# Kernel optimization log

Measured on AMD Instinct MI355X. Metric: run time of the kernel, lower is better.

The kernel has to match this reference:

```python
import jax, jax.numpy as jnp
import numpy as np

HEADS = 16  # matches init_kwargs


def setup_inputs() -> dict:
    key = jax.random.key(0)
    ks = jax.random.split(key, 9)
    N, L, E, D = 2, 2048, 1024, 64
    return {
        "query": jax.random.normal(ks[0], (N, L, E), dtype=jnp.float32),
        "keys": jax.random.normal(ks[1], (N, L, E), dtype=jnp.float32),
        "values": jax.random.normal(ks[2], (N, L, E), dtype=jnp.float32),
        "masks": jax.random.randint(ks[3], (N, 1, 1, L), 0, 2, dtype=jnp.int32),
        "Wq": jax.random.normal(ks[4], (D, D), dtype=jnp.float32) / np.sqrt(D),
        "Wk": jax.random.normal(ks[5], (D, D), dtype=jnp.float32) / np.sqrt(D),
        "Wv": jax.random.normal(ks[6], (D, D), dtype=jnp.float32) / np.sqrt(D),
        "Wo": jax.random.normal(ks[7], (E, E), dtype=jnp.float32) / np.sqrt(E),
        "bo": jax.random.normal(ks[8], (E,), dtype=jnp.float32),
    }


def reference(query, keys, values, masks, Wq, Wk, Wv, Wo, bo):
    N, Lq, E = query.shape
    Lk = keys.shape[1]
    H = HEADS
    D = E // H
    # split heads: [N, L, H, D]
    q = query.reshape(N, Lq, H, D)
    k = keys.reshape(N, Lk, H, D)
    v = values.reshape(N, Lk, H, D)
    # per-head linear projections (weights shared across heads); Linear: x @ W.T
    q = jnp.einsum("nqhd,ed->nqhe", q, Wq)
    k = jnp.einsum("nkhd,ed->nkhe", k, Wk)
    v = jnp.einsum("nkhd,ed->nkhe", v, Wv)
    # scores [N, H, Lq, Lk]
    scores = jnp.einsum("nqhd,nkhd->nhqk", q, k)
    scores = jnp.where(masks == 0, jnp.float32(-1e20), scores)
    # NOTE: original scales by sqrt(embed_size), not sqrt(head_dim)
    attn = jax.nn.softmax(scores / jnp.sqrt(jnp.float32(E)), axis=3)
    out = jnp.einsum("nhqk,nkhd->nqhd", attn, v).reshape(N, Lq, E)
    return out @ Wo.T + bo
```

## Files before the change

kernel.cpp:

```cpp
#include <hip/hip_runtime.h>


typedef __bf16 bf16_t;
typedef __bf16 bf16x4 __attribute__((ext_vector_type(4)));
typedef __bf16 bf16x8 __attribute__((ext_vector_type(8)));
typedef float f32x4 __attribute__((ext_vector_type(4)));

#define MFMA16(a, b, c) __builtin_amdgcn_mfma_f32_16x16x32_bf16((a), (b), (c), 0, 0, 0)

#define GLOAD_LDS16(gp, lp)                                              \
    __builtin_amdgcn_global_load_lds(                                    \
        (const __attribute__((address_space(1))) void*)(gp),             \
        (__attribute__((address_space(3))) void*)(lp), 16, 0, 0)

__device__ inline bf16x8 cvt8(const float* __restrict__ p, float scale) {
    f32x4 a = *(const f32x4*)p;
    f32x4 b = *(const f32x4*)(p + 4);
    bf16x8 r;
    r[0] = (bf16_t)(a[0] * scale); r[1] = (bf16_t)(a[1] * scale);
    r[2] = (bf16_t)(a[2] * scale); r[3] = (bf16_t)(a[3] * scale);
    r[4] = (bf16_t)(b[0] * scale); r[5] = (bf16_t)(b[1] * scale);
    r[6] = (bf16_t)(b[2] * scale); r[7] = (bf16_t)(b[3] * scale);
    return r;
}

__global__ __launch_bounds__(256) void scan_kernel(const int* __restrict__ msk,
                                                   int* __restrict__ excl)
{
    __shared__ int sums[256];
    const int t = threadIdx.x;
    for (int n = 0; n < 2; n++) {
        const int* m = msk + n * 2048;
        int* e = excl + n * 2049;
        int v[8], s = 0;
        #pragma unroll
        for (int j = 0; j < 8; j++) { v[j] = (m[t * 8 + j] != 0); s += v[j]; }
        sums[t] = s;
        __syncthreads();
        if (t == 0) {
            int a = 0;
            for (int i = 0; i < 256; i++) { int x = sums[i]; sums[i] = a; a += x; }
            e[2048] = a;
        }
        __syncthreads();
        int a = sums[t];
        #pragma unroll
        for (int j = 0; j < 8; j++) { e[t * 8 + j] = a; a += v[j]; }
        __syncthreads();
    }
}

__global__ __launch_bounds__(256) void qkv_proj_kernel(
    const float* __restrict__ qin, const float* __restrict__ kin,
    const float* __restrict__ vin,
    const float* __restrict__ Wq, const float* __restrict__ Wk,
    const float* __restrict__ Wv, const float* __restrict__ Wo,
    const int* __restrict__ excl,
    bf16_t* __restrict__ qp, bf16_t* __restrict__ kc, bf16_t* __restrict__ vcT,
    bf16_t* __restrict__ Wob)
{
    __shared__ __align__(16) char smem[51200];

    const int t = threadIdx.x;
    const int w = t >> 6, lane = t & 63, quad = lane >> 4, l16 = lane & 15;

    if (blockIdx.y == 3) {
        int idx = blockIdx.x * 1024 + t * 4;
        f32x4 v = *(const f32x4*)&Wo[idx];
        bf16x4 r;
        r[0] = (bf16_t)v[0]; r[1] = (bf16_t)v[1];
        r[2] = (bf16_t)v[2]; r[3] = (bf16_t)v[3];
        *(bf16x4*)&Wob[idx] = r;
        return;
    }

    if (blockIdx.y == 2) {
        bf16_t* Ct = (bf16_t*)smem;
        short* mapS = (short*)(smem + 16384);
        const int h = blockIdx.x & 15;
        const int tb = (blockIdx.x >> 4) * 64;
        const int n = tb >> 11, l0 = tb & 2047;
        const int tg = tb + w * 16 + l16;

        bf16x8 b0 = cvt8(&vin[(size_t)tg * 1024 + h * 64 + quad * 8], 1.0f);
        bf16x8 b1 = cvt8(&vin[(size_t)tg * 1024 + h * 64 + 32 + quad * 8], 1.0f);

        const int cbase = excl[n * 2049 + l0];
        const int cnt   = excl[n * 2049 + l0 + 64] - cbase;
        if (t < 64) {
            int c  = excl[n * 2049 + l0 + t];
            int c1 = excl[n * 2049 + l0 + t + 1];
            if (c1 > c) mapS[c - cbase] = (short)t;
        }

        #pragma unroll
        for (int nt = 0; nt < 4; nt++) {
            bf16x8 a0 = cvt8(&Wv[(nt * 16 + l16) * 64 + quad * 8], 1.0f);
            bf16x8 a1 = cvt8(&Wv[(nt * 16 + l16) * 64 + 32 + quad * 8], 1.0f);
            f32x4 acc = {0.f, 0.f, 0.f, 0.f};
            acc = MFMA16(a0, b0, acc);
            acc = MFMA16(a1, b1, acc);
            #pragma unroll
            for (int r = 0; r < 4; r++)
                Ct[(nt * 16 + quad * 4 + r) * 72 + w * 16 + l16] = (bf16_t)acc[r];
        }
        __syncthreads();
        const int p = t & 63, rg = t >> 6;
        if (p < cnt) {
            int j = mapS[p];
            size_t ob = ((size_t)(n * 16 + h)) * 131072 + cbase + p;
            #pragma unroll
            for (int rr = 0; rr < 16; rr++) {
                int r = rg * 16 + rr;
                vcT[ob + (size_t)r * 2048] = Ct[r * 72 + j];
            }
        }
        return;
    }

    if (blockIdx.x >= 512) return;
    const bool isK = (blockIdx.y == 1);
    const float* x; const float* W; float scale;
    if (!isK) { x = qin; W = Wq; scale = 0.03125f; }
    else      { x = kin; W = Wk; scale = 1.0f; }

    float* Xs = (float*)smem;
    bf16_t* Ct2 = (bf16_t*)(smem + 32768);

    const int g0 = blockIdx.x * 128;

    #pragma unroll
    for (int j = 0; j < 8; j++) {
        int br = w * 32 + j * 4;
        GLOAD_LDS16(&x[(size_t)(g0 + br) * 64 + lane * 4], &Xs[br * 64]);
    }
    __syncthreads();

    const int rbase = w * 32;
    bf16x8 a[2][2];
    #pragma unroll
    for (int qs = 0; qs < 2; qs++)
        #pragma unroll
        for (int c = 0; c < 2; c++)
            a[qs][c] = cvt8(&Xs[(rbase + qs * 16 + l16) * 64 + c * 32 + quad * 8], scale);

    f32x4 acc[4][2];
    #pragma unroll
    for (int nt = 0; nt < 4; nt++) {
        bf16x8 b0 = cvt8(&W[(nt * 16 + l16) * 64 + quad * 8], 1.0f);
        bf16x8 b1 = cvt8(&W[(nt * 16 + l16) * 64 + 32 + quad * 8], 1.0f);
        #pragma unroll
        for (int qs = 0; qs < 2; qs++) {
            f32x4 z = {0.f, 0.f, 0.f, 0.f};
            z = MFMA16(a[qs][0], b0, z);
            z = MFMA16(a[qs][1], b1, z);
            acc[nt][qs] = z;
        }
    }

    #pragma unroll
    for (int nt = 0; nt < 4; nt++)
        #pragma unroll
        for (int qs = 0; qs < 2; qs++)
            #pragma unroll
            for (int r = 0; r < 4; r++)
                Ct2[(rbase + qs * 16 + quad * 4 + r) * 72 + nt * 16 + l16] = (bf16_t)acc[nt][qs][r];
    __syncthreads();

    #pragma unroll
    for (int it = 0; it < 4; it++) {
        int j = it * 32 + (t >> 3);
        int g = g0 + j, h2 = g & 15, token = g >> 4;
        int n2 = token >> 11, l = token & 2047;
        bf16x8 val = *(const bf16x8*)&Ct2[j * 72 + (t & 7) * 8];
        if (isK) {
            int c  = excl[n2 * 2049 + l];
            int c1 = excl[n2 * 2049 + l + 1];
            if (c1 > c)
                *(bf16x8*)&kc[(((size_t)(n2 * 16 + h2)) * 2048 + c) * 64 + (t & 7) * 8] = val;
        } else {
            *(bf16x8*)&qp[(((size_t)(n2 * 16 + h2)) * 2048 + l) * 64 + (t & 7) * 8] = val;
        }
    }
}

__global__ __launch_bounds__(256) void attn_kernel(
    const bf16_t* __restrict__ qp, const bf16_t* __restrict__ kc,
    const bf16_t* __restrict__ vcT, const int* __restrict__ excl,
    bf16_t* __restrict__ ao)
{
    __shared__ bf16_t Kt[2][64][64];
    __shared__ bf16_t Vt[2][64][64];
    __shared__ bf16_t PwT[4][32][72];

    const int t = threadIdx.x;
    const int w = t >> 6, lane = t & 63, quad = lane >> 4, l16 = lane & 15;

    const int flat = blockIdx.x;
    const int xcd = flat & 7, slot = flat >> 3;
    const int nh = xcd * 4 + (slot >> 4), qb = slot & 15;
    const int n = nh >> 4, h = nh & 15;
    const int qbase = qb * 128 + w * 32;
    const size_t nhbase = (size_t)nh * 131072;

    const int Lc = excl[n * 2049 + 2048];
    const int ntiles = (Lc + 63) >> 6;

    bf16x8 aq[2][2];
    #pragma unroll
    for (int qs = 0; qs < 2; qs++)
        #pragma unroll
        for (int c = 0; c < 2; c++)
            aq[qs][c] = *(const bf16x8*)&qp[nhbase + (size_t)(qbase + qs * 16 + l16) * 64 + c * 32 + quad * 8];

    f32x4 o[2][4];
    float lsum[2] = {0.f, 0.f};
    #pragma unroll
    for (int qs = 0; qs < 2; qs++)
        #pragma unroll
        for (int dt = 0; dt < 4; dt++) {
            o[qs][dt][0] = 0.f; o[qs][dt][1] = 0.f; o[qs][dt][2] = 0.f; o[qs][dt][3] = 0.f;
        }

    const int kwbase = w * 16;

    #pragma unroll
    for (int j = 0; j < 2; j++) {
        int rb = kwbase + j * 8;
        GLOAD_LDS16(&kc[nhbase + (size_t)rb * 64 + lane * 8], &Kt[0][rb][0]);
        GLOAD_LDS16(&vcT[nhbase + (size_t)(rb + (lane >> 3)) * 2048 + (lane & 7) * 8],
                    &Vt[0][rb][0]);
    }

    for (int i = 0; i < ntiles; i++) {
        const int cb = i & 1, nb = cb ^ 1;
        const int k0 = i * 64;
        __syncthreads();

        if (i + 1 < ntiles) {
            const int kn = k0 + 64;
            #pragma unroll
            for (int j = 0; j < 2; j++) {
                int rb = kwbase + j * 8;
                GLOAD_LDS16(&kc[nhbase + (size_t)(kn + rb) * 64 + lane * 8], &Kt[nb][rb][0]);
                GLOAD_LDS16(&vcT[nhbase + (size_t)(rb + (lane >> 3)) * 2048 + kn + (lane & 7) * 8],
                            &Vt[nb][rb][0]);
            }
        }

        f32x4 st[2][4];
        #pragma unroll
        for (int ct = 0; ct < 4; ct++) {
            bf16x8 kb0 = *(const bf16x8*)&Kt[cb][ct * 16 + l16][quad * 8];
            bf16x8 kb1 = *(const bf16x8*)&Kt[cb][ct * 16 + l16][32 + quad * 8];
            #pragma unroll
            for (int qs = 0; qs < 2; qs++) {
                f32x4 acc = {0.f, 0.f, 0.f, 0.f};
                acc = MFMA16(kb0, aq[qs][0], acc);
                acc = MFMA16(kb1, aq[qs][1], acc);
                st[qs][ct] = acc;
            }
        }

        if (k0 + 64 <= Lc) {
            #pragma unroll
            for (int ct = 0; ct < 4; ct++)
                #pragma unroll
                for (int qs = 0; qs < 2; qs++) {
                    bf16x4 pk;
                    #pragma unroll
                    for (int r = 0; r < 4; r++) {
                        float p = __expf(st[qs][ct][r]);
                        lsum[qs] += p;
                        pk[r] = (bf16_t)p;
                    }
                    *(bf16x4*)&PwT[w][qs * 16 + l16][ct * 16 + quad * 4] = pk;
                }
        } else {
            #pragma unroll
            for (int ct = 0; ct < 4; ct++)
                #pragma unroll
                for (int qs = 0; qs < 2; qs++) {
                    bf16x4 pk;
                    #pragma unroll
                    for (int r = 0; r < 4; r++) {
                        int kk = k0 + ct * 16 + quad * 4 + r;
                        float p = (kk < Lc) ? __expf(st[qs][ct][r]) : 0.0f;
                        lsum[qs] += p;
                        pk[r] = (bf16_t)p;
                    }
                    *(bf16x4*)&PwT[w][qs * 16 + l16][ct * 16 + quad * 4] = pk;
                }
        }
        asm volatile("s_waitcnt lgkmcnt(0)" ::: "memory");

        bf16x8 bp[2][2];
        #pragma unroll
        for (int qs = 0; qs < 2; qs++) {
            bp[qs][0] = *(const bf16x8*)&PwT[w][qs * 16 + l16][quad * 8];
            bp[qs][1] = *(const bf16x8*)&PwT[w][qs * 16 + l16][32 + quad * 8];
        }
        #pragma unroll
        for (int dt = 0; dt < 4; dt++) {
            bf16x8 va0 = *(const bf16x8*)&Vt[cb][dt * 16 + l16][quad * 8];
            bf16x8 va1 = *(const bf16x8*)&Vt[cb][dt * 16 + l16][32 + quad * 8];
            #pragma unroll
            for (int qs = 0; qs < 2; qs++) {
                o[qs][dt] = MFMA16(va0, bp[qs][0], o[qs][dt]);
                o[qs][dt] = MFMA16(va1, bp[qs][1], o[qs][dt]);
            }
        }
    }

    #pragma unroll
    for (int qs = 0; qs < 2; qs++) {
        float v = lsum[qs];
        v += __shfl_xor(v, 16);
        v += __shfl_xor(v, 32);
        float inv = 1.0f / v;
        const int q = qbase + qs * 16 + l16;
        const size_t base = ((size_t)n * 2048 + q) * 1024 + h * 64;
        #pragma unroll
        for (int dt = 0; dt < 4; dt++) {
            bf16x4 ov;
            #pragma unroll
            for (int r = 0; r < 4; r++) ov[r] = (bf16_t)(o[qs][dt][r] * inv);
            *(bf16x4*)&ao[base + dt * 16 + quad * 4] = ov;
        }
    }
}

__global__ __launch_bounds__(256, 2) void out_proj_kernel(
    const bf16_t* __restrict__ X, const bf16_t* __restrict__ Wob,
    const float* __restrict__ bo, float* __restrict__ out)
{
    __shared__ bf16_t Xs[2][128][64];
    __shared__ bf16_t Ws[2][64][64];

    const int t = threadIdx.x;
    const int w = t >> 6, lane = t & 63, quad = lane >> 4, l16 = lane & 15;
    const int Mbase = blockIdx.x * 128;
    const int Nbase = blockIdx.y * 64;
    const int mrow = (w & 1) * 64;
    const int ncol = (w >> 1) * 32;

    f32x4 acc[4][2];
    #pragma unroll
    for (int mi = 0; mi < 4; mi++)
        #pragma unroll
        for (int ni = 0; ni < 2; ni++) {
            acc[mi][ni][0] = 0.f; acc[mi][ni][1] = 0.f;
            acc[mi][ni][2] = 0.f; acc[mi][ni][3] = 0.f;
        }

    #pragma unroll
    for (int j = 0; j < 4; j++) {
        int br = w * 32 + j * 8;
        GLOAD_LDS16(&X[(size_t)(Mbase + br + (lane >> 3)) * 1024 + (lane & 7) * 8],
                    &Xs[0][br][0]);
    }
    #pragma unroll
    for (int j = 0; j < 2; j++) {
        int br = w * 16 + j * 8;
        GLOAD_LDS16(&Wob[(size_t)(Nbase + br + (lane >> 3)) * 1024 + (lane & 7) * 8],
                    &Ws[0][br][0]);
    }

    for (int i = 0; i < 16; i++) {
        const int cb = i & 1, nb = cb ^ 1;
        __syncthreads();

        if (i < 15) {
            const int kn = (i + 1) * 64;
            #pragma unroll
            for (int j = 0; j < 4; j++) {
                int br = w * 32 + j * 8;
                GLOAD_LDS16(&X[(size_t)(Mbase + br + (lane >> 3)) * 1024 + kn + (lane & 7) * 8],
                            &Xs[nb][br][0]);
            }
            #pragma unroll
            for (int j = 0; j < 2; j++) {
                int br = w * 16 + j * 8;
                GLOAD_LDS16(&Wob[(size_t)(Nbase + br + (lane >> 3)) * 1024 + kn + (lane & 7) * 8],
                            &Ws[nb][br][0]);
            }
        }

        #pragma unroll
        for (int c = 0; c < 2; c++) {
            bf16x8 bfr[2];
            #pragma unroll
            for (int ni = 0; ni < 2; ni++)
                bfr[ni] = *(const bf16x8*)&Ws[cb][ncol + ni * 16 + l16][c * 32 + quad * 8];
            #pragma unroll
            for (int mi = 0; mi < 4; mi++) {
                bf16x8 afr = *(const bf16x8*)&Xs[cb][mrow + mi * 16 + l16][c * 32 + quad * 8];
                #pragma unroll
                for (int ni = 0; ni < 2; ni++)
                    acc[mi][ni] = MFMA16(afr, bfr[ni], acc[mi][ni]);
            }
        }
    }

    #pragma unroll
    for (int ni = 0; ni < 2; ni++) {
        float b = bo[Nbase + ncol + ni * 16 + l16];
        #pragma unroll
        for (int mi = 0; mi < 4; mi++) {
            #pragma unroll
            for (int r = 0; r < 4; r++) {
                int row = Mbase + mrow + mi * 16 + quad * 4 + r;
                out[(size_t)row * 1024 + Nbase + ncol + ni * 16 + l16] = acc[mi][ni][r] + b;
            }
        }
    }
}

extern "C" void kernel_launch(void* const* d_in, const int* in_sizes, int n_in,
                              void* d_out, int out_size, void* d_ws, size_t ws_size,
                              hipStream_t stream)
{
    const float* qin = (const float*)d_in[0];
    const float* kin = (const float*)d_in[1];
    const float* vin = (const float*)d_in[2];
    const int*   msk = (const int*)d_in[3];
    const float* Wq  = (const float*)d_in[4];
    const float* Wk  = (const float*)d_in[5];
    const float* Wv  = (const float*)d_in[6];
    const float* Wo  = (const float*)d_in[7];
    const float* bo  = (const float*)d_in[8];
    float* out = (float*)d_out;

    bf16_t* ws  = (bf16_t*)d_ws;
    bf16_t* qp  = ws;
    bf16_t* kc  = ws + 4194304;
    bf16_t* vcT = ws + 8388608;
    bf16_t* ao  = ws + 12582912;
    bf16_t* Wob = ws + 16777216;
    int* excl   = (int*)(ws + 17825792);

    scan_kernel<<<1, 256, 0, stream>>>(msk, excl);
    qkv_proj_kernel<<<dim3(1024, 4), 256, 0, stream>>>(qin, kin, vin, Wq, Wk, Wv, Wo,
                                                        excl, qp, kc, vcT, Wob);
    attn_kernel<<<dim3(512), 256, 0, stream>>>(qp, kc, vcT, excl, ao);
    out_proj_kernel<<<dim3(32, 16), 256, 0, stream>>>(ao, Wob, bo, out);
}
```

Measured before the change: 184.5 us.

## Keep softmax probabilities in registers via permlane swaps, use exp2, parallelize mask scan

The attention kernel no longer writes P through an LDS staging buffer. It packs probabilities to bf16 with v_cvt_pk_bf16_f32 and rearranges them across lane quads with permlane32/16 swaps so they can feed the PV MFMA directly. The Q scale now folds in log2(e), so raw v_exp_f32 (exp2) replaces __expf. The mask prefix-scan runs on one block per batch and uses a wave shuffle scan instead of a serial 256-element loop. The change removes LDS traffic and waits in the inner loop, but it depends on the permlane swaps reproducing the exact operand layout the MFMA expects.

```diff
diff --git a/kernel.cpp b/kernel.cpp
--- a/kernel.cpp
+++ b/kernel.cpp
@@ -5,6 +5,7 @@
 typedef __bf16 bf16x4 __attribute__((ext_vector_type(4)));
 typedef __bf16 bf16x8 __attribute__((ext_vector_type(8)));
 typedef float f32x4 __attribute__((ext_vector_type(4)));
+typedef unsigned int u32x4 __attribute__((ext_vector_type(4)));
 
 #define MFMA16(a, b, c) __builtin_amdgcn_mfma_f32_16x16x32_bf16((a), (b), (c), 0, 0, 0)
 
@@ -24,30 +25,54 @@
     return r;
 }
 
+__device__ inline float exp2_fast(float x) {
+    float r;
+    asm("v_exp_f32 %0, %1" : "=v"(r) : "v"(x));
+    return r;
+}
+
+__device__ inline unsigned cvt_pk_bf16(float lo, float hi) {
+    unsigned r;
+    asm("v_cvt_pk_bf16_f32 %0, %1, %2" : "=v"(r) : "v"(lo), "v"(hi));
+    return r;
+}
+
+__device__ inline void xchg_quads(unsigned &x, unsigned &y) {
+    asm("v_permlane32_swap_b32 %0, %1\n\t"
+        "v_permlane16_swap_b32 %0, %1"
+        : "+v"(x), "+v"(y));
+}
+
 __global__ __launch_bounds__(256) void scan_kernel(const int* __restrict__ msk,
                                                    int* __restrict__ excl)
 {
-    __shared__ int sums[256];
-    const int t = threadIdx.x;
-    for (int n = 0; n < 2; n++) {
-        const int* m = msk + n * 2048;
-        int* e = excl + n * 2049;
-        int v[8], s = 0;
-        #pragma unroll
-        for (int j = 0; j < 8; j++) { v[j] = (m[t * 8 + j] != 0); s += v[j]; }
-        sums[t] = s;
-        __syncthreads();
-        if (t == 0) {
-            int a = 0;
-            for (int i = 0; i < 256; i++) { int x = sums[i]; sums[i] = a; a += x; }
-            e[2048] = a;
-        }
-        __syncthreads();
-        int a = sums[t];
-        #pragma unroll
-        for (int j = 0; j < 8; j++) { e[t * 8 + j] = a; a += v[j]; }
-        __syncthreads();
-    }
+    __shared__ int wsum[4];
+    const int n = blockIdx.x;
+    const int t = threadIdx.x, lane = t & 63, w = t >> 6;
+    const int* m = msk + n * 2048;
+    int* e = excl + n * 2049;
+
+    int v[8], s = 0;
+    #pragma unroll
+    for (int j = 0; j < 8; j++) { v[j] = (m[t * 8 + j] != 0); s += v[j]; }
+
+    int inc = s;
+    #pragma unroll
+    for (int d = 1; d < 64; d <<= 1) {
+        int o = __shfl_up(inc, d);
+        if (lane >= d) inc += o;
+    }
+    if (lane == 63) wsum[w] = inc;
+    __syncthreads();
+    int off = 0;
+    #pragma unroll
+    for (int i = 0; i < 4; i++)
+        if (i < w) off += wsum[i];
+
+    int a = off + inc - s;
+    #pragma unroll
+    for (int j = 0; j < 8; j++) { e[t * 8 + j] = a; a += v[j]; }
+    if (t == 255) e[2048] = a;
 }
 
 __global__ __launch_bounds__(256) void qkv_proj_kernel(
@@ -121,7 +146,7 @@
     if (blockIdx.x >= 512) return;
     const bool isK = (blockIdx.y == 1);
     const float* x; const float* W; float scale;
-    if (!isK) { x = qin; W = Wq; scale = 0.03125f; }
+    if (!isK) { x = qin; W = Wq; scale = 0.04508422f; }
     else      { x = kin; W = Wk; scale = 1.0f; }
 
     float* Xs = (float*)smem;
@@ -191,7 +216,6 @@
 {
     __shared__ bf16_t Kt[2][64][64];
     __shared__ bf16_t Vt[2][64][64];
-    __shared__ bf16_t PwT[4][32][72];
 
     const int t = threadIdx.x;
     const int w = t >> 6, lane = t & 63, quad = lane >> 4, l16 = lane & 15;
@@ -264,42 +288,49 @@
 
         if (k0 + 64 <= Lc) {
             #pragma unroll
-            for (int ct = 0; ct < 4; ct++)
+            for (int qs = 0; qs < 2; qs++)
                 #pragma unroll
-                for (int qs = 0; qs < 2; qs++) {
-                    bf16x4 pk;
+                for (int ct = 0; ct < 4; ct++)
                     #pragma unroll
                     for (int r = 0; r < 4; r++) {
-                        float p = __expf(st[qs][ct][r]);
+                        float p = exp2_fast(st[qs][ct][r]);
                         lsum[qs] += p;
-                        pk[r] = (bf16_t)p;
+                        st[qs][ct][r] = p;
                     }
-                    *(bf16x4*)&PwT[w][qs * 16 + l16][ct * 16 + quad * 4] = pk;
-                }
         } else {
             #pragma unroll
-            for (int ct = 0; ct < 4; ct++)
+            for (int qs = 0; qs < 2; qs++)
                 #pragma unroll
-                for (int qs = 0; qs < 2; qs++) {
-                    bf16x4 pk;
+                for (int ct = 0; ct < 4; ct++)
                     #pragma unroll
                     for (int r = 0; r < 4; r++) {
                         int kk = k0 + ct * 16 + quad * 4 + r;
-                        float p = (kk < Lc) ? __expf(st[qs][ct][r]) : 0.0f;
+                        float p = (kk < Lc) ? exp2_fast(st[qs][ct][r]) : 0.0f;
                         lsum[qs] += p;
-                        pk[r] = (bf16_t)p;
+                        st[qs][ct][r] = p;
                     }
-                    *(bf16x4*)&PwT[w][qs * 16 + l16][ct * 16 + quad * 4] = pk;
-                }
-        }
-        asm volatile("s_waitcnt lgkmcnt(0)" ::: "memory");
+        }
 
         bf16x8 bp[2][2];
         #pragma unroll
         for (int qs = 0; qs < 2; qs++) {
-            bp[qs][0] = *(const bf16x8*)&PwT[w][qs * 16 + l16][quad * 8];
-            bp[qs][1] = *(const bf16x8*)&PwT[w][qs * 16 + l16][32 + quad * 8];
-        }
+            unsigned u[4][2];
+            #pragma unroll
+            for (int ct = 0; ct < 4; ct++) {
+                u[ct][0] = cvt_pk_bf16(st[qs][ct][0], st[qs][ct][1]);
+                u[ct][1] = cvt_pk_bf16(st[qs][ct][2], st[qs][ct][3]);
+            }
+            #pragma unroll
+            for (int hh = 0; hh < 2; hh++) {
+                unsigned b0 = u[2 * hh][0], b2 = u[2 * hh + 1][0];
+                xchg_quads(b0, b2);
+                unsigned b1 = u[2 * hh][1], b3 = u[2 * hh + 1][1];
+                xchg_quads(b1, b3);
+                u32x4 q4 = {b0, b1, b2, b3};
+                bp[qs][hh] = __builtin_bit_cast(bf16x8, q4);
+            }
+        }
+
         #pragma unroll
         for (int dt = 0; dt < 4; dt++) {
             bf16x8 va0 = *(const bf16x8*)&Vt[cb][dt * 16 + l16][quad * 8];
@@ -439,7 +470,7 @@
     bf16_t* Wob = ws + 16777216;
     int* excl   = (int*)(ws + 17825792);
 
-    scan_kernel<<<1, 256, 0, stream>>>(msk, excl);
+    scan_kernel<<<2, 256, 0, stream>>>(msk, excl);
     qkv_proj_kernel<<<dim3(1024, 4), 256, 0, stream>>>(qin, kin, vin, Wq, Wk, Wv, Wo,
                                                         excl, qp, kc, vcT, Wob);
     attn_kernel<<<dim3(512), 256, 0, stream>>>(qp, kc, vcT, excl, ao);
```

New measurement: 178.4 us. 3.3% less time.
